# Kernel tuning notes

Hardware: AMD Instinct MI355X
Metric: run time of the kernel (lower is better)

The kernel has to match this reference:

```python
import jax, jax.numpy as jnp
import numpy as np

K_MASK = jnp.finfo(jnp.bfloat16).min
ROPE_THETA = 1000000.0


def _rope_sincos(position_ids, head_dim, theta):
    # position_ids: [b, t] int -> sin, cos: [b, t, head_dim//2]
    frac = jnp.arange(0, head_dim, 2, dtype=jnp.float32) / head_dim
    timescale = theta ** frac
    ang = position_ids[..., None].astype(jnp.float32) / timescale
    return jnp.sin(ang), jnp.cos(ang)


def _apply_rope(x, sin, cos):
    # x: [b, t, n, h]; sin/cos: [b, t, h//2]
    h = x.shape[-1]
    x1, x2 = x[..., : h // 2], x[..., h // 2 :]
    s = sin[:, :, None, :]
    c = cos[:, :, None, :]
    return jnp.concatenate([x1 * c - x2 * s, x2 * c + x1 * s], axis=-1).astype(x.dtype)


def setup_inputs() -> dict:
    key = jax.random.key(0)
    ks = jax.random.split(key, 8)
    b, t, S = 8, 16, 8192
    D, N, K, H = 1536, 12, 2, 128
    std = 0.01  # nnx.initializers.normal() default stddev
    return {
        "x": jax.random.normal(ks[0], (b, t, D), jnp.float32),
        "k_cache": jax.random.normal(ks[1], (b, S, K, H), jnp.float32),
        "v_cache": jax.random.normal(ks[2], (b, S, K, H), jnp.float32),
        "wq": jax.random.normal(ks[3], (D, N, H), jnp.float32) * std,
        "bq": jnp.zeros((N, H), jnp.float32),
        "wk": jax.random.normal(ks[4], (D, K, H), jnp.float32) * std,
        "bk": jnp.zeros((K, H), jnp.float32),
        "wv": jax.random.normal(ks[5], (D, K, H), jnp.float32) * std,
        "bv": jnp.zeros((K, H), jnp.float32),
        "wo": jax.random.normal(ks[6], (N, H, D), jnp.float32) * std,
        "segment_ids": jnp.ones((b, t), jnp.int32),
        "start_ind": jnp.zeros((8,), jnp.int32),
        "cur_ind": 4096,
    }


def reference(x, k_cache, v_cache, wq, bq, wk, bk, wv, bv, wo,
              segment_ids, start_ind, cur_ind):
    b, t, D = x.shape
    S = k_cache.shape[1]
    N, H = wq.shape[1], wq.shape[2]
    K = wk.shape[1]
    G = N // K  # n_rep
    scale = H ** -0.5

    # projections with bias
    q = jnp.einsum("btd,dnh->btnh", x, wq) + bq
    kp = jnp.einsum("btd,dkh->btkh", x, wk) + bk
    v = jnp.einsum("btd,dkh->btkh", x, wv) + bv

    # left-pad bookkeeping (count_left_pads) and start index resolution
    nonpad = segment_ids != 0  # [b, t]
    left_pads = jnp.argmax(nonpad, axis=-1).astype(jnp.int32)
    start = jnp.where(start_ind < 0, left_pads, start_ind)  # [b]

    # positions from segment ids, offset by current cache index
    positions = jnp.maximum(jnp.cumsum(nonpad.astype(jnp.int32), axis=-1) - 1, 0) + cur_ind
    sin, cos = _rope_sincos(positions, H, ROPE_THETA)
    q = _apply_rope(q, sin, cos)
    kp = _apply_rope(kp, sin, cos)

    # cache update
    k_cache = jax.lax.dynamic_update_slice(k_cache, kp.astype(k_cache.dtype), (0, cur_ind, 0, 0))
    v_cache = jax.lax.dynamic_update_slice(v_cache, v.astype(v_cache.dtype), (0, cur_ind, 0, 0))

    # GQA attention over full cache
    qg = q.reshape(b, t, K, G, H)
    logits = jnp.einsum("btkgh,bskh->btskg", qg, k_cache) * scale  # [b,t,S,K,G]

    q_pos = cur_ind + jnp.arange(t, dtype=jnp.int32)[None, :] - start[:, None]  # [b,t]
    ts = jnp.arange(S, dtype=jnp.int32)
    kv_seg = (ts[None, :] >= start[:, None]) & (ts[None, :] < cur_ind + t)  # [b,S]
    k_pos = ts[None, :] - start[:, None]
    causal = k_pos[:, None, :] <= q_pos[:, :, None]  # [b,t,S]
    seg = kv_seg[:, None, :].astype(segment_ids.dtype) == segment_ids[:, :, None]  # [b,t,S]
    mask = (causal & seg)[:, :, :, None, None]

    logits = jnp.where(mask, logits, K_MASK)
    w = jax.nn.softmax(logits.astype(jnp.float32), axis=2).astype(logits.dtype)
    qkv = jnp.einsum("btskg,bskh->btkgh", w, v_cache).reshape(b, t, N, H)
    return jnp.einsum("btnh,nhd->btd", qkv, wo)
```

## Files before the change

kernel.cpp:

```cpp
#include <hip/hip_runtime.h>
#include <hip/hip_bf16.h>

#define B_ 8
#define T_ 16
#define D_ 1536
#define N_ 12
#define KH_ 2
#define G_ 6
#define H_ 128
#define S_ 8192
#define NCHUNK 16
#define SPLITS 8

typedef __attribute__((ext_vector_type(8))) short bf16x8;
typedef __attribute__((ext_vector_type(4))) float f32x4;
typedef __attribute__((ext_vector_type(4))) unsigned short u16x4;

__device__ __forceinline__ unsigned short f2bf(float x) {
    unsigned u = __float_as_uint(x);
    u += 0x7fffu + ((u >> 16) & 1u);
    return (unsigned short)(u >> 16);
}
__device__ __forceinline__ float bf2f(unsigned short h) {
    return __uint_as_float(((unsigned)h) << 16);
}

__device__ __forceinline__ void gload16(const float* g, void* l) {
    __builtin_amdgcn_global_load_lds(
        (const __attribute__((address_space(1))) unsigned int*)g,
        (__attribute__((address_space(3))) unsigned int*)l,
        16, 0, 0);
}

__global__ __launch_bounds__(256, 4) void gemm_splitk(
    const float* __restrict__ A,
    const float* __restrict__ W0, int n0, int ldb0,
    const float* __restrict__ W1, int n1, int ldb1,
    const float* __restrict__ W2, int ldb2,
    float* __restrict__ part, int NTOT, int Kdim)
{
    __shared__ __align__(16) unsigned short Ah[64][40], Al[64][40];
    __shared__ __align__(16) unsigned short Bh[64][40], Bl[64][40];
    const int tid = threadIdx.x;
    const int wave = tid >> 6, lane = tid & 63;
    const int col = lane & 15, g = lane >> 4;
    const int row0 = blockIdx.y * 64;
    const int c0 = blockIdx.x * 64;
    const int ks = Kdim / gridDim.z;
    const int k0 = blockIdx.z * ks;

    const float* Bp; int ldb, bc0;
    if (c0 < n0)           { Bp = W0; ldb = ldb0; bc0 = c0; }
    else if (c0 < n0 + n1) { Bp = W1; ldb = ldb1; bc0 = c0 - n0; }
    else                   { Bp = W2; ldb = ldb2; bc0 = c0 - n0 - n1; }

    f32x4 acc[4];
#pragma unroll
    for (int nt = 0; nt < 4; ++nt) acc[nt] = (f32x4){0.f, 0.f, 0.f, 0.f};

    for (int kk = 0; kk < ks; kk += 32) {
        __syncthreads();
        if (tid < 128) {
#pragma unroll
            for (int c = tid; c < 512; c += 128) {
                int r = c >> 3, k4 = c & 7;
                float4 v = *(const float4*)&A[(size_t)(row0 + r) * Kdim + k0 + kk + k4 * 4];
                float f[4] = {v.x, v.y, v.z, v.w};
                u16x4 hv, lv;
#pragma unroll
                for (int i = 0; i < 4; ++i) {
                    unsigned short hh = f2bf(f[i]);
                    hv[i] = hh; lv[i] = f2bf(f[i] - bf2f(hh));
                }
                *(u16x4*)&Ah[r][k4 * 4] = hv;
                *(u16x4*)&Al[r][k4 * 4] = lv;
            }
        } else {
            int t2 = tid - 128;
            int kq = t2 >> 4, cq = t2 & 15;
            float a[4][4];
#pragma unroll
            for (int r = 0; r < 4; ++r) {
                float4 v = *(const float4*)&Bp[(size_t)(k0 + kk + kq * 4 + r) * ldb + bc0 + cq * 4];
                a[r][0] = v.x; a[r][1] = v.y; a[r][2] = v.z; a[r][3] = v.w;
            }
#pragma unroll
            for (int cc = 0; cc < 4; ++cc) {
                u16x4 hv, lv;
#pragma unroll
                for (int r = 0; r < 4; ++r) {
                    unsigned short hh = f2bf(a[r][cc]);
                    hv[r] = hh; lv[r] = f2bf(a[r][cc] - bf2f(hh));
                }
                *(u16x4*)&Bh[cq * 4 + cc][kq * 4] = hv;
                *(u16x4*)&Bl[cq * 4 + cc][kq * 4] = lv;
            }
        }
        __syncthreads();

        bf16x8 ah = *(const bf16x8*)&Ah[wave * 16 + col][g * 8];
        bf16x8 al = *(const bf16x8*)&Al[wave * 16 + col][g * 8];
#pragma unroll
        for (int nt = 0; nt < 4; ++nt) {
            bf16x8 bh = *(const bf16x8*)&Bh[nt * 16 + col][g * 8];
            bf16x8 bl = *(const bf16x8*)&Bl[nt * 16 + col][g * 8];
            acc[nt] = __builtin_amdgcn_mfma_f32_16x16x32_bf16(ah, bh, acc[nt], 0, 0, 0);
            acc[nt] = __builtin_amdgcn_mfma_f32_16x16x32_bf16(ah, bl, acc[nt], 0, 0, 0);
            acc[nt] = __builtin_amdgcn_mfma_f32_16x16x32_bf16(al, bh, acc[nt], 0, 0, 0);
        }
    }
#pragma unroll
    for (int nt = 0; nt < 4; ++nt)
#pragma unroll
        for (int j = 0; j < 4; ++j) {
            size_t prow = (size_t)blockIdx.z * 128 + row0 + wave * 16 + g * 4 + j;
            part[prow * NTOT + c0 + nt * 16 + col] = acc[nt][j];
        }
}

__global__ __launch_bounds__(256) void rope_reduce(
    const float* __restrict__ part,
    const float* __restrict__ bq, const float* __restrict__ bk,
    const float* __restrict__ bv,
    const int* __restrict__ seg, const int* __restrict__ curp,
    float* __restrict__ q_rope, float* __restrict__ k_new,
    float* __restrict__ v_new)
{
    const int row = blockIdx.x;
    const int b = row >> 4, t = row & 15;
    const int tid = threadIdx.x;
    __shared__ float S[2048];
    __shared__ float sc[64][2];

    const int CUR = curp[0];
    int c = 0;
    for (int tt = 0; tt <= t; ++tt) c += (seg[b * T_ + tt] != 0) ? 1 : 0;
    int pos = max(c - 1, 0) + CUR;

    if (tid < 64) {
        float frac = (2.0f * tid) / (float)H_;
        float ts = expf(frac * logf(1000000.0f));
        float ang = (float)pos / ts;
        sc[tid][0] = sinf(ang);
        sc[tid][1] = cosf(ang);
    }
    for (int e = tid; e < 2048; e += 256) {
        float s = 0.f;
#pragma unroll
        for (int sp = 0; sp < SPLITS; ++sp)
            s += part[((size_t)sp * 128 + row) * 2048 + e];
        S[e] = s;
    }
    __syncthreads();

    for (int e = tid; e < 768; e += 256) {
        int n = e >> 6, i = e & 63;
        float x1 = S[n * 128 + i] + bq[n * 128 + i];
        float x2 = S[n * 128 + i + 64] + bq[n * 128 + i + 64];
        float s = sc[i][0], co = sc[i][1];
        q_rope[(size_t)row * 1536 + n * 128 + i]      = x1 * co - x2 * s;
        q_rope[(size_t)row * 1536 + n * 128 + i + 64] = x2 * co + x1 * s;
    }
    if (tid < 128) {
        int n = tid >> 6, i = tid & 63;
        float x1 = S[1536 + n * 128 + i] + bk[n * 128 + i];
        float x2 = S[1536 + n * 128 + i + 64] + bk[n * 128 + i + 64];
        float s = sc[i][0], co = sc[i][1];
        k_new[(size_t)row * 256 + n * 128 + i]      = x1 * co - x2 * s;
        k_new[(size_t)row * 256 + n * 128 + i + 64] = x2 * co + x1 * s;
    }
    v_new[(size_t)row * 256 + tid] = S[1792 + tid] + bv[tid];
}

__global__ __launch_bounds__(384, 3) void attn_mfma(
    const float* __restrict__ q_rope, const float* __restrict__ k_new,
    const float* __restrict__ v_new,
    const float* __restrict__ k_cache, const float* __restrict__ v_cache,
    const int* __restrict__ seg, const int* __restrict__ start_ind,
    const int* __restrict__ curp,
    float* __restrict__ part)
{
    const int chunk = blockIdx.x, b = blockIdx.y, kh = blockIdx.z;
    const int tid = threadIdx.x;
    const int wave = tid >> 6, lane = tid & 63;
    const int col = lane & 15, g = lane >> 4;
    const float scale = 0.088388347648318447f;
    const float NEG_INF = -__builtin_inff();

    const int CUR = curp[0];
    const int SPAN = CUR + T_;
    const int CH = (SPAN + NCHUNK - 1) / NCHUNK;
    const int s0 = chunk * CH;
    const int s1 = min(s0 + CH, SPAN);

    int st = start_ind[b];
    if (st < 0) {
        st = 0;
        for (int tt = 0; tt < T_; ++tt)
            if (seg[b * T_ + tt] != 0) { st = tt; break; }
    }

    __shared__ __align__(16) float Ksw[2][32][128];
    __shared__ __align__(16) unsigned short Vt[2][128][40];
    __shared__ __align__(16) unsigned short Pl[6][16][40];

    const int qbase = wave * 16;
    const int qi_a = qbase + col;
    const int t_a = (qi_a * 171) >> 10;
    const int gh_a = qi_a - t_a * G_;
    const float* qp = &q_rope[(((size_t)b * T_ + t_a) * N_ + kh * G_ + gh_a) * H_];
    bf16x8 qf[4];
#pragma unroll
    for (int ks = 0; ks < 4; ++ks) {
        float4 va = *(const float4*)&qp[ks * 32 + g * 8];
        float4 vb = *(const float4*)&qp[ks * 32 + g * 8 + 4];
        float f[8] = {va.x, va.y, va.z, va.w, vb.x, vb.y, vb.z, vb.w};
        union { bf16x8 v; __hip_bfloat162 h2[4]; } W;
#pragma unroll
        for (int i = 0; i < 4; ++i)
            W.h2[i] = __float22bfloat162_rn(make_float2(f[2 * i] * scale, f[2 * i + 1] * scale));
        qf[ks] = W.v;
    }

    int qpos_r[4], segid_r[4];
#pragma unroll
    for (int j = 0; j < 4; ++j) {
        int qi_c = qbase + g * 4 + j;
        int t_c = (qi_c * 171) >> 10;
        segid_r[j] = seg[b * T_ + t_c];
        qpos_r[j] = CUR + t_c - st;
    }

    float m[4], lsum[4];
#pragma unroll
    for (int j = 0; j < 4; ++j) { m[j] = NEG_INF; lsum[j] = 0.f; }
    f32x4 oacc[8];
#pragma unroll
    for (int nt = 0; nt < 8; ++nt) oacc[nt] = (f32x4){0.f, 0.f, 0.f, 0.f};

    auto krow = [&](int s) -> const float* {
        s = min(s, SPAN - 1);
        return (s < CUR)
            ? &k_cache[((((size_t)b * S_ + s) * KH_) + kh) * H_]
            : &k_new[((((size_t)b * T_ + (s - CUR)) * KH_) + kh) * H_];
    };
    auto vrow = [&](int s) -> const float* {
        s = min(s, SPAN - 1);
        return (s < CUR)
            ? &v_cache[((((size_t)b * S_ + s) * KH_) + kh) * H_]
            : &v_new[((((size_t)b * T_ + (s - CUR)) * KH_) + kh) * H_];
    };

    auto stageK = [&](int bufi, int stile) {
#pragma unroll
        for (int i = 0; i < 3; ++i) {
            int idx = tid + i * 384;
            if (idx < 1024) {
                int row = idx >> 5, s = idx & 31;
                int sg = s ^ (row & 7);
                gload16(krow(stile + row) + sg * 4, &Ksw[bufi][row][s * 4]);
            }
        }
    };
    const int vky4 = tid >> 5, vd4 = tid & 31;
    auto loadV = [&](float4* vreg, int stile) {
        if (tid < 256) {
#pragma unroll
            for (int r = 0; r < 4; ++r)
                vreg[r] = *(const float4*)(vrow(stile + vky4 * 4 + r) + vd4 * 4);
        }
    };
    auto writeV = [&](int bufi, const float4* vreg) {
        if (tid < 256) {
            float a[4][4];
#pragma unroll
            for (int r = 0; r < 4; ++r) {
                a[r][0] = vreg[r].x; a[r][1] = vreg[r].y;
                a[r][2] = vreg[r].z; a[r][3] = vreg[r].w;
            }
#pragma unroll
            for (int dd = 0; dd < 4; ++dd) {
                u16x4 hv;
#pragma unroll
                for (int r = 0; r < 4; ++r) hv[r] = f2bf(a[r][dd]);
                *(u16x4*)&Vt[bufi][vd4 * 4 + dd][vky4 * 4] = hv;
            }
        }
    };

    auto computeTile = [&](int bufi, int stile) {
        f32x4 sacc0 = {0.f, 0.f, 0.f, 0.f}, sacc1 = {0.f, 0.f, 0.f, 0.f};
#pragma unroll
        for (int kt = 0; kt < 2; ++kt) {
            const int row = kt * 16 + col;
            const int rx = row & 7;
#pragma unroll
            for (int ks = 0; ks < 4; ++ks) {
                const int sl = ks * 8 + g * 2;
                float4 a = *(const float4*)&Ksw[bufi][row][(sl ^ rx) * 4];
                float4 bb = *(const float4*)&Ksw[bufi][row][((sl + 1) ^ rx) * 4];
                float f[8] = {a.x, a.y, a.z, a.w, bb.x, bb.y, bb.z, bb.w};
                union { bf16x8 v; __hip_bfloat162 h2[4]; } W;
#pragma unroll
                for (int i = 0; i < 4; ++i)
                    W.h2[i] = __float22bfloat162_rn(make_float2(f[2 * i], f[2 * i + 1]));
                if (kt == 0)
                    sacc0 = __builtin_amdgcn_mfma_f32_16x16x32_bf16(qf[ks], W.v, sacc0, 0, 0, 0);
                else
                    sacc1 = __builtin_amdgcn_mfma_f32_16x16x32_bf16(qf[ks], W.v, sacc1, 0, 0, 0);
            }
        }

        float rj[4];
        const int skey0 = stile + col, skey1 = stile + 16 + col;
#pragma unroll
        for (int j = 0; j < 4; ++j) {
            bool v0 = (skey0 < s1) && (skey0 - st <= qpos_r[j]) &&
                      (((skey0 >= st) ? 1 : 0) == segid_r[j]);
            bool v1 = (skey1 < s1) && (skey1 - st <= qpos_r[j]) &&
                      (((skey1 >= st) ? 1 : 0) == segid_r[j]);
            float lg0 = v0 ? sacc0[j] : NEG_INF;
            float lg1 = v1 ? sacc1[j] : NEG_INF;
            float tm = fmaxf(lg0, lg1);
            tm = fmaxf(tm, __shfl_xor(tm, 1));
            tm = fmaxf(tm, __shfl_xor(tm, 2));
            tm = fmaxf(tm, __shfl_xor(tm, 4));
            tm = fmaxf(tm, __shfl_xor(tm, 8));
            float mn = fmaxf(m[j], tm);
            float r, p0, p1;
            if (mn == NEG_INF) { r = 1.f; p0 = 0.f; p1 = 0.f; }
            else {
                r  = __expf(m[j] - mn);
                p0 = __expf(lg0 - mn);
                p1 = __expf(lg1 - mn);
            }
            float ps = p0 + p1;
            ps += __shfl_xor(ps, 1);
            ps += __shfl_xor(ps, 2);
            ps += __shfl_xor(ps, 4);
            ps += __shfl_xor(ps, 8);
            lsum[j] = lsum[j] * r + ps;
            m[j] = mn;
            rj[j] = r;
            int row = g * 4 + j;
            Pl[wave][row][col]      = f2bf(p0);
            Pl[wave][row][16 + col] = f2bf(p1);
        }

#pragma unroll
        for (int nt = 0; nt < 8; ++nt) {
#pragma unroll
            for (int j = 0; j < 4; ++j) oacc[nt][j] *= rj[j];
        }

        bf16x8 pa = *(const bf16x8*)&Pl[wave][col][g * 8];
#pragma unroll
        for (int nt = 0; nt < 8; ++nt) {
            bf16x8 vb = *(const bf16x8*)&Vt[bufi][nt * 16 + col][g * 8];
            oacc[nt] = __builtin_amdgcn_mfma_f32_16x16x32_bf16(pa, vb, oacc[nt], 0, 0, 0);
        }
    };

    const int ntiles = (s1 - s0 + 31) >> 5;
    float4 vA[4], vB[4];
    stageK(0, s0);
    loadV(vA, s0);
    writeV(0, vA);
    __syncthreads();

    for (int ti = 0; ti < ntiles; ti += 2) {
        if (ti + 1 < ntiles) { stageK(1, s0 + (ti + 1) * 32); loadV(vB, s0 + (ti + 1) * 32); }
        computeTile(0, s0 + ti * 32);
        if (ti + 1 < ntiles) writeV(1, vB);
        __syncthreads();
        if (ti + 1 < ntiles) {
            if (ti + 2 < ntiles) { stageK(0, s0 + (ti + 2) * 32); loadV(vA, s0 + (ti + 2) * 32); }
            computeTile(1, s0 + (ti + 1) * 32);
            if (ti + 2 < ntiles) writeV(0, vA);
            __syncthreads();
        }
    }

    const size_t base_q = (((size_t)chunk * B_ + b) * KH_ + kh) * 96;
#pragma unroll
    for (int j = 0; j < 4; ++j) {
        int qi = qbase + g * 4 + j;
        size_t pb = (base_q + qi) * 132;
        if (col == 0) { part[pb] = m[j]; part[pb + 1] = lsum[j]; }
#pragma unroll
        for (int nt = 0; nt < 8; ++nt)
            part[pb + 2 + nt * 16 + col] = oacc[nt][j];
    }
}

__global__ __launch_bounds__(256) void combine_kernel(
    const float* __restrict__ part, float* __restrict__ qkv)
{
    const int row = blockIdx.x;
    const int b = row >> 4, t = row & 15;
    const int tid = threadIdx.x;
    const int half = tid >> 7, h = tid & 127;
    const size_t cstride = (size_t)B_ * KH_ * 96 * 132;

    for (int nb = 0; nb < N_; nb += 2) {
        int n = nb + half;
        int kh = n / G_, g = n - kh * G_;
        int qi = t * G_ + g;
        size_t base0 = (((size_t)b * KH_ + kh) * 96 + qi) * 132;
        float M = -__builtin_inff();
        for (int c = 0; c < NCHUNK; ++c)
            M = fmaxf(M, part[base0 + c * cstride]);
        float den = 0.f, num = 0.f;
        for (int c = 0; c < NCHUNK; ++c) {
            float mc = part[base0 + c * cstride];
            float e = (M == -__builtin_inff() || mc == -__builtin_inff())
                          ? 0.f : expf(mc - M);
            den += e * part[base0 + c * cstride + 1];
            num += e * part[base0 + c * cstride + 2 + h];
        }
        qkv[(size_t)row * (N_ * H_) + n * H_ + h] = (den > 0.f) ? num / den : 0.f;
    }
}

__global__ __launch_bounds__(256) void sum_reduce(
    const float* __restrict__ part, float* __restrict__ out, int n)
{
    int i = blockIdx.x * 256 + threadIdx.x;
    if (i < n) {
        float s = 0.f;
#pragma unroll
        for (int sp = 0; sp < SPLITS; ++sp) s += part[(size_t)sp * n + i];
        out[i] = s;
    }
}

extern "C" void kernel_launch(void* const* d_in, const int* in_sizes, int n_in,
                              void* d_out, int out_size, void* d_ws, size_t ws_size,
                              hipStream_t stream)
{
    (void)in_sizes; (void)n_in; (void)out_size; (void)ws_size;
    const float* x       = (const float*)d_in[0];
    const float* k_cache = (const float*)d_in[1];
    const float* v_cache = (const float*)d_in[2];
    const float* wq      = (const float*)d_in[3];
    const float* bq      = (const float*)d_in[4];
    const float* wk      = (const float*)d_in[5];
    const float* bk      = (const float*)d_in[6];
    const float* wv      = (const float*)d_in[7];
    const float* bv      = (const float*)d_in[8];
    const float* wo      = (const float*)d_in[9];
    const int*   seg     = (const int*)d_in[10];
    const int*   start_i = (const int*)d_in[11];
    const int*   curp    = (const int*)d_in[12];
    float* out = (float*)d_out;
    float* ws  = (float*)d_ws;

    const size_t PSZ  = (size_t)NCHUNK * B_ * KH_ * 96 * 132;
    const size_t QSZ  = (size_t)B_ * T_ * N_ * H_;
    const size_t KSZ  = (size_t)B_ * T_ * KH_ * H_;
    float* partP  = ws;
    float* partA  = ws;
    float* q_rope = ws + PSZ;
    float* k_new  = q_rope + QSZ;
    float* v_new  = k_new + KSZ;
    float* qkv    = v_new + KSZ;

    gemm_splitk<<<dim3(32, 2, SPLITS), 256, 0, stream>>>(
        x, wq, 1536, 1536, wk, 256, 256, wv, 256, partP, 2048, D_);

    rope_reduce<<<B_ * T_, 256, 0, stream>>>(partP, bq, bk, bv, seg, curp,
                                             q_rope, k_new, v_new);

    attn_mfma<<<dim3(NCHUNK, B_, KH_), 384, 0, stream>>>(
        q_rope, k_new, v_new, k_cache, v_cache, seg, start_i, curp, partA);

    combine_kernel<<<B_ * T_, 256, 0, stream>>>(partA, qkv);

    gemm_splitk<<<dim3(24, 2, SPLITS), 256, 0, stream>>>(
        qkv, wo, 1536, 1536, wo, 0, 1536, wo, 1536, partP, 1536, N_ * H_);

    sum_reduce<<<(B_ * T_ * D_ + 255) / 256, 256, 0, stream>>>(
        partP, out, B_ * T_ * D_);
}
```

Measured before the change: 96.49 us.

## Load K directly from global into registers and double attention chunks

Drops the LDS staging of K tiles (global_load_lds plus a swizzled shared buffer). Each wave now reads its K rows straight from global memory into registers inside the compute step. It also doubles the number of sequence chunks to raise grid parallelism, and relaxes the launch-bounds occupancy hint. The trade-off: all six waves re-read the same K rows from global or L2 instead of sharing one LDS copy, and those loads are no longer prefetched ahead of compute, so their latency is exposed. The combine stage must also merge twice as many partial results.

```diff
diff --git a/kernel.cpp b/kernel.cpp
--- a/kernel.cpp
+++ b/kernel.cpp
@@ -9,7 +9,7 @@
 #define G_ 6
 #define H_ 128
 #define S_ 8192
-#define NCHUNK 16
+#define NCHUNK 32
 #define SPLITS 8
 
 typedef __attribute__((ext_vector_type(8))) short bf16x8;
@@ -23,13 +23,6 @@
 }
 __device__ __forceinline__ float bf2f(unsigned short h) {
     return __uint_as_float(((unsigned)h) << 16);
-}
-
-__device__ __forceinline__ void gload16(const float* g, void* l) {
-    __builtin_amdgcn_global_load_lds(
-        (const __attribute__((address_space(1))) unsigned int*)g,
-        (__attribute__((address_space(3))) unsigned int*)l,
-        16, 0, 0);
 }
 
 __global__ __launch_bounds__(256, 4) void gemm_splitk(
@@ -172,7 +165,7 @@
     v_new[(size_t)row * 256 + tid] = S[1792 + tid] + bv[tid];
 }
 
-__global__ __launch_bounds__(384, 3) void attn_mfma(
+__global__ __launch_bounds__(384) void attn_mfma(
     const float* __restrict__ q_rope, const float* __restrict__ k_new,
     const float* __restrict__ v_new,
     const float* __restrict__ k_cache, const float* __restrict__ v_cache,
@@ -200,7 +193,6 @@
             if (seg[b * T_ + tt] != 0) { st = tt; break; }
     }
 
-    __shared__ __align__(16) float Ksw[2][32][128];
     __shared__ __align__(16) unsigned short Vt[2][128][40];
     __shared__ __align__(16) unsigned short Pl[6][16][40];
 
@@ -251,17 +243,6 @@
             : &v_new[((((size_t)b * T_ + (s - CUR)) * KH_) + kh) * H_];
     };
 
-    auto stageK = [&](int bufi, int stile) {
-#pragma unroll
-        for (int i = 0; i < 3; ++i) {
-            int idx = tid + i * 384;
-            if (idx < 1024) {
-                int row = idx >> 5, s = idx & 31;
-                int sg = s ^ (row & 7);
-                gload16(krow(stile + row) + sg * 4, &Ksw[bufi][row][s * 4]);
-            }
-        }
-    };
     const int vky4 = tid >> 5, vd4 = tid & 31;
     auto loadV = [&](float4* vreg, int stile) {
         if (tid < 256) {
@@ -289,26 +270,31 @@
     };
 
     auto computeTile = [&](int bufi, int stile) {
+        const float* kr0 = krow(stile + col);
+        const float* kr1 = krow(stile + 16 + col);
+        float4 kfa[8], kfb[8];
+#pragma unroll
+        for (int ks = 0; ks < 4; ++ks) {
+            kfa[ks * 2 + 0] = *(const float4*)(kr0 + ks * 32 + g * 8);
+            kfa[ks * 2 + 1] = *(const float4*)(kr0 + ks * 32 + g * 8 + 4);
+            kfb[ks * 2 + 0] = *(const float4*)(kr1 + ks * 32 + g * 8);
+            kfb[ks * 2 + 1] = *(const float4*)(kr1 + ks * 32 + g * 8 + 4);
+        }
         f32x4 sacc0 = {0.f, 0.f, 0.f, 0.f}, sacc1 = {0.f, 0.f, 0.f, 0.f};
 #pragma unroll
-        for (int kt = 0; kt < 2; ++kt) {
-            const int row = kt * 16 + col;
-            const int rx = row & 7;
-#pragma unroll
-            for (int ks = 0; ks < 4; ++ks) {
-                const int sl = ks * 8 + g * 2;
-                float4 a = *(const float4*)&Ksw[bufi][row][(sl ^ rx) * 4];
-                float4 bb = *(const float4*)&Ksw[bufi][row][((sl + 1) ^ rx) * 4];
-                float f[8] = {a.x, a.y, a.z, a.w, bb.x, bb.y, bb.z, bb.w};
-                union { bf16x8 v; __hip_bfloat162 h2[4]; } W;
-#pragma unroll
-                for (int i = 0; i < 4; ++i)
-                    W.h2[i] = __float22bfloat162_rn(make_float2(f[2 * i], f[2 * i + 1]));
-                if (kt == 0)
-                    sacc0 = __builtin_amdgcn_mfma_f32_16x16x32_bf16(qf[ks], W.v, sacc0, 0, 0, 0);
-                else
-                    sacc1 = __builtin_amdgcn_mfma_f32_16x16x32_bf16(qf[ks], W.v, sacc1, 0, 0, 0);
-            }
+        for (int ks = 0; ks < 4; ++ks) {
+            float fa[8] = {kfa[ks*2].x, kfa[ks*2].y, kfa[ks*2].z, kfa[ks*2].w,
+                           kfa[ks*2+1].x, kfa[ks*2+1].y, kfa[ks*2+1].z, kfa[ks*2+1].w};
+            float fb[8] = {kfb[ks*2].x, kfb[ks*2].y, kfb[ks*2].z, kfb[ks*2].w,
+                           kfb[ks*2+1].x, kfb[ks*2+1].y, kfb[ks*2+1].z, kfb[ks*2+1].w};
+            union { bf16x8 v; __hip_bfloat162 h2[4]; } Wa, Wb;
+#pragma unroll
+            for (int i = 0; i < 4; ++i) {
+                Wa.h2[i] = __float22bfloat162_rn(make_float2(fa[2 * i], fa[2 * i + 1]));
+                Wb.h2[i] = __float22bfloat162_rn(make_float2(fb[2 * i], fb[2 * i + 1]));
+            }
+            sacc0 = __builtin_amdgcn_mfma_f32_16x16x32_bf16(qf[ks], Wa.v, sacc0, 0, 0, 0);
+            sacc1 = __builtin_amdgcn_mfma_f32_16x16x32_bf16(qf[ks], Wb.v, sacc1, 0, 0, 0);
         }
 
         float rj[4];
@@ -363,18 +349,17 @@
 
     const int ntiles = (s1 - s0 + 31) >> 5;
     float4 vA[4], vB[4];
-    stageK(0, s0);
     loadV(vA, s0);
     writeV(0, vA);
     __syncthreads();
 
     for (int ti = 0; ti < ntiles; ti += 2) {
-        if (ti + 1 < ntiles) { stageK(1, s0 + (ti + 1) * 32); loadV(vB, s0 + (ti + 1) * 32); }
+        if (ti + 1 < ntiles) loadV(vB, s0 + (ti + 1) * 32);
         computeTile(0, s0 + ti * 32);
         if (ti + 1 < ntiles) writeV(1, vB);
         __syncthreads();
         if (ti + 1 < ntiles) {
-            if (ti + 2 < ntiles) { stageK(0, s0 + (ti + 2) * 32); loadV(vA, s0 + (ti + 2) * 32); }
+            if (ti + 2 < ntiles) loadV(vA, s0 + (ti + 2) * 32);
             computeTile(1, s0 + (ti + 1) * 32);
             if (ti + 2 < ntiles) writeV(0, vA);
             __syncthreads();
```

Result: slower. 172.8 us (+79.0%).
